# Performance work log

Hardware: AMD Instinct MI355X
Metric: run time of the kernel (lower is better)

## Reference

```python
import jax, jax.numpy as jnp
import numpy as np

S, B, H = 4096, 32, 512

def setup_inputs() -> dict:
    key = jax.random.key(0)
    k1, k2, k3, k4, k5 = jax.random.split(key, 5)
    hidden = jax.random.normal(k1, (1, B, H), dtype=jnp.float32)
    encoder_outputs = jax.random.normal(k2, (S, B, H), dtype=jnp.float32)
    embedding = jax.random.normal(k3, (S, B, 3), dtype=jnp.float32)
    # learned params (xavier-ish scale)
    bigram_matrix = jax.random.normal(k4, (H, H), dtype=jnp.float32) * (1.0 / np.sqrt(H))
    affect_matrix = jax.random.normal(k5, (H, 3), dtype=jnp.float32) * 0.1
    return {"hidden": hidden, "encoder_outputs": encoder_outputs,
            "embedding": embedding, "bigram_matrix": bigram_matrix,
            "affect_matrix": affect_matrix}

def reference(hidden, encoder_outputs, embedding, bigram_matrix, affect_matrix):
    # hidden: [1,B,H] -> [B,H] (view(-1) over single layer)
    h = hidden[0]
    # bigram-modulated encoder states:
    #   i == 0: enc[0]
    #   i  > 0: (enc[i-1] @ W_bigram) * enc[i]
    modulated = jnp.einsum('sbh,hk->sbk', encoder_outputs[:-1], bigram_matrix) * encoder_outputs[1:]
    bigram_hidden = jnp.concatenate([encoder_outputs[:1], modulated], axis=0)  # [S,B,H]
    # dot-attention energy per (b, s)
    e_dot = jnp.einsum('sbh,bh->bs', bigram_hidden, h)  # [B,S]
    # affect term: (h @ affect_matrix) . embedding[s,b]
    e_aff = jnp.einsum('bk,sbk->bs', jnp.einsum('bh,hk->bk', h, affect_matrix), embedding)
    attn = jax.nn.softmax(e_dot + e_aff, axis=-1)  # softmax over seq dim
    return attn[:, None, :]  # [B,1,S]
```

## Files before the change

### kernel.cpp

```cpp
#include <hip/hip_runtime.h>
#include <cstdint>
#include <cstddef>

#define S_DIM 4096
#define B_DIM 32
#define H_DIM 512
#define M_DIM (S_DIM * B_DIM)

typedef unsigned short u16;
typedef unsigned int u32;
typedef float f32x4 __attribute__((ext_vector_type(4)));
typedef __bf16 bf16x8 __attribute__((ext_vector_type(8)));

__device__ __forceinline__ u16 f2bf(float v) {
    union { float f; u32 u; } a; a.f = v;
    u32 r = a.u + 0x7fffu + ((a.u >> 16) & 1u);
    return (u16)(r >> 16);
}
__device__ __forceinline__ float bf2f(u16 b) {
    union { float f; u32 u; } a; a.u = ((u32)b) << 16; return a.f;
}
__device__ __forceinline__ void split_bf(float v, u16& h, u16& l) {
    h = f2bf(v);
    l = f2bf(v - bf2f(h));
}

__device__ __forceinline__ void gl2lds16(const void* g, void* l) {
    __builtin_amdgcn_global_load_lds(
        (const __attribute__((address_space(1))) unsigned int*)g,
        (__attribute__((address_space(3))) unsigned int*)l,
        16, 0, 0);
}

__global__ void prep_w(const float* __restrict__ W,
                       u16* __restrict__ Wh, u16* __restrict__ Wl) {
    int i = blockIdx.x * 256 + threadIdx.x;
    float w = W[i];
    u16 h, l;
    split_bf(w, h, l);
    Wh[i] = h; Wl[i] = l;
}

__global__ void prep_v(const float* __restrict__ enc,
                       const float* __restrict__ hid,
                       u16* __restrict__ vh, u16* __restrict__ vl,
                       int m_base, int m_count) {
    const size_t nq = (size_t)m_count * (H_DIM / 4);
    const size_t stride = (size_t)gridDim.x * 256;
    for (size_t i = blockIdx.x * 256 + threadIdx.x; i < nq; i += stride) {
        const size_t elem  = i * 4;
        const size_t gelem = (size_t)m_base * H_DIM + elem;
        const int k = (int)(gelem & (H_DIM - 1));
        const int b = (int)((gelem >> 9) & 31);
        const float4 e = *(const float4*)(enc + gelem);
        const float4 h = *(const float4*)(hid + b * H_DIM + k);
        float v0 = e.x * h.x, v1 = e.y * h.y, v2 = e.z * h.z, v3 = e.w * h.w;
        u16 h0,h1,h2,h3,l0,l1,l2,l3;
        split_bf(v0, h0, l0); split_bf(v1, h1, l1);
        split_bf(v2, h2, l2); split_bf(v3, h3, l3);
        ushort4 hw, lw;
        hw.x = h0; hw.y = h1; hw.z = h2; hw.w = h3;
        lw.x = l0; lw.y = l1; lw.z = l2; lw.w = l3;
        *(ushort4*)(vh + elem) = hw;
        *(ushort4*)(vl + elem) = lw;
    }
}

__global__ __launch_bounds__(256, 2) void bigram_gemm(
    const float* __restrict__ enc,
    const u16* __restrict__ vh, const u16* __restrict__ vl,
    const u16* __restrict__ Wh, const u16* __restrict__ Wl,
    float* __restrict__ Lp, int m_base)
{
    __shared__ u16 sAh[128 * 32];
    __shared__ u16 sAl[128 * 32];
    __shared__ u16 sBh[128 * 32];
    __shared__ u16 sBl[128 * 32];
    __shared__ float rowsum[2][128];

    const int tid  = threadIdx.x;
    const int wave = tid >> 6;
    const int lane = tid & 63;
    const int wr   = wave >> 1;
    const int wc   = wave & 1;
    const int jt   = blockIdx.x & 3;
    const int mt   = blockIdx.x >> 2;
    const int m0   = m_base + mt * 128;
    const int j0   = jt * 128;
    const int g    = lane >> 4;
    const int cl   = lane & 15;

    const int srow = wave * 32 + (lane >> 2);
    const int scol = (lane & 3) * 8;
    const size_t aoff0 = (size_t)(mt * 128 + srow) * H_DIM + scol;
    const size_t aoff1 = aoff0 + (size_t)16 * H_DIM;
    const size_t boff0 = (size_t)(j0 + srow) * H_DIM + scol;
    const size_t boff1 = boff0 + (size_t)16 * H_DIM;
    const u16* pAh0 = vh + aoff0; const u16* pAh1 = vh + aoff1;
    const u16* pAl0 = vl + aoff0; const u16* pAl1 = vl + aoff1;
    const u16* pBh0 = Wh + boff0; const u16* pBh1 = Wh + boff1;
    const u16* pBl0 = Wl + boff0; const u16* pBl1 = Wl + boff1;
    const int d0 = wave * 1024, d1 = wave * 1024 + 512;

    f32x4 acc[4][4];
    #pragma unroll
    for (int mf = 0; mf < 4; ++mf)
        #pragma unroll
        for (int nf = 0; nf < 4; ++nf)
            acc[mf][nf] = (f32x4){0.f, 0.f, 0.f, 0.f};

    for (int kt = 0; kt < 16; ++kt) {
        const int ko = kt * 32;
        __syncthreads();
        gl2lds16(pAh0 + ko, sAh + d0);
        gl2lds16(pAh1 + ko, sAh + d1);
        gl2lds16(pAl0 + ko, sAl + d0);
        gl2lds16(pAl1 + ko, sAl + d1);
        gl2lds16(pBh0 + ko, sBh + d0);
        gl2lds16(pBh1 + ko, sBh + d1);
        gl2lds16(pBl0 + ko, sBl + d0);
        gl2lds16(pBl1 + ko, sBl + d1);
        __syncthreads();

        bf16x8 ah[4], al[4], bh[4], bl[4];
        #pragma unroll
        for (int mf = 0; mf < 4; ++mf) {
            const int ar = wr * 64 + mf * 16 + cl;
            ah[mf] = *(const bf16x8*)(sAh + ar * 32 + g * 8);
            al[mf] = *(const bf16x8*)(sAl + ar * 32 + g * 8);
        }
        #pragma unroll
        for (int nf = 0; nf < 4; ++nf) {
            const int br = wc * 64 + nf * 16 + cl;
            bh[nf] = *(const bf16x8*)(sBh + br * 32 + g * 8);
            bl[nf] = *(const bf16x8*)(sBl + br * 32 + g * 8);
        }
        #pragma unroll
        for (int mf = 0; mf < 4; ++mf)
            #pragma unroll
            for (int nf = 0; nf < 4; ++nf) {
                acc[mf][nf] = __builtin_amdgcn_mfma_f32_16x16x32_bf16(ah[mf], bh[nf], acc[mf][nf], 0, 0, 0);
                acc[mf][nf] = __builtin_amdgcn_mfma_f32_16x16x32_bf16(ah[mf], bl[nf], acc[mf][nf], 0, 0, 0);
                acc[mf][nf] = __builtin_amdgcn_mfma_f32_16x16x32_bf16(al[mf], bh[nf], acc[mf][nf], 0, 0, 0);
            }
    }

    #pragma unroll
    for (int mf = 0; mf < 4; ++mf) {
        float rs0 = 0.f, rs1 = 0.f, rs2 = 0.f, rs3 = 0.f;
        const int growb = m0 + wr * 64 + mf * 16 + g * 4;
        #pragma unroll
        for (int nf = 0; nf < 4; ++nf) {
            const int gcol = j0 + wc * 64 + nf * 16 + cl;
            float e0 = (growb + 0 >= B_DIM) ? enc[(size_t)(growb + 0 - B_DIM) * H_DIM + gcol] : 0.f;
            float e1 = (growb + 1 >= B_DIM) ? enc[(size_t)(growb + 1 - B_DIM) * H_DIM + gcol] : 0.f;
            float e2 = (growb + 2 >= B_DIM) ? enc[(size_t)(growb + 2 - B_DIM) * H_DIM + gcol] : 0.f;
            float e3 = (growb + 3 >= B_DIM) ? enc[(size_t)(growb + 3 - B_DIM) * H_DIM + gcol] : 0.f;
            rs0 += acc[mf][nf][0] * e0;
            rs1 += acc[mf][nf][1] * e1;
            rs2 += acc[mf][nf][2] * e2;
            rs3 += acc[mf][nf][3] * e3;
        }
        #pragma unroll
        for (int off = 1; off < 16; off <<= 1) {
            rs0 += __shfl_xor(rs0, off);
            rs1 += __shfl_xor(rs1, off);
            rs2 += __shfl_xor(rs2, off);
            rs3 += __shfl_xor(rs3, off);
        }
        if (cl == 0) {
            const int rb = wr * 64 + mf * 16 + g * 4;
            rowsum[wc][rb + 0] = rs0;
            rowsum[wc][rb + 1] = rs1;
            rowsum[wc][rb + 2] = rs2;
            rowsum[wc][rb + 3] = rs3;
        }
    }
    __syncthreads();
    if (tid < 128) {
        const int gm = m0 + tid;
        if (gm >= B_DIM) {
            Lp[(size_t)jt * M_DIM + (size_t)(gm & 31) * S_DIM + (gm >> 5)] =
                rowsum[0][tid] + rowsum[1][tid];
        }
    }
}

__global__ __launch_bounds__(256, 2) void bigram_gemm_direct(
    const float* __restrict__ enc,
    const float* __restrict__ hid,
    const u16* __restrict__ Wh,
    const u16* __restrict__ Wl,
    float* __restrict__ Lp)
{
    __shared__ float rowsum[2][128];
    const int tid  = threadIdx.x;
    const int wave = tid >> 6;
    const int lane = tid & 63;
    const int wr   = wave >> 1;
    const int wc   = wave & 1;
    const int jt   = blockIdx.x & 3;
    const int m0   = (blockIdx.x >> 2) * 128;
    const int j0   = jt * 128;
    const int g    = lane >> 4;
    const int cl   = lane & 15;

    f32x4 acc[4][4];
    #pragma unroll
    for (int mf = 0; mf < 4; ++mf)
        #pragma unroll
        for (int nf = 0; nf < 4; ++nf)
            acc[mf][nf] = (f32x4){0.f, 0.f, 0.f, 0.f};

    for (int kt = 0; kt < 8; ++kt) {
        #pragma unroll
        for (int kk = 0; kk < 2; ++kk) {
            const int k0 = kt * 64 + kk * 32 + g * 8;
            const float4 hA0 = *(const float4*)(hid + (size_t)cl * H_DIM + k0);
            const float4 hA1 = *(const float4*)(hid + (size_t)cl * H_DIM + k0 + 4);
            const float4 hB0 = *(const float4*)(hid + (size_t)(cl + 16) * H_DIM + k0);
            const float4 hB1 = *(const float4*)(hid + (size_t)(cl + 16) * H_DIM + k0 + 4);
            bf16x8 ah[4], al[4];
            #pragma unroll
            for (int mf = 0; mf < 4; ++mf) {
                const size_t rbase = (size_t)(m0 + wr * 64 + mf * 16 + cl) * H_DIM + k0;
                const float4 e0 = *(const float4*)(enc + rbase);
                const float4 e1 = *(const float4*)(enc + rbase + 4);
                const float4 h0 = (mf & 1) ? hB0 : hA0;
                const float4 h1 = (mf & 1) ? hB1 : hA1;
                float v[8];
                v[0] = e0.x * h0.x; v[1] = e0.y * h0.y; v[2] = e0.z * h0.z; v[3] = e0.w * h0.w;
                v[4] = e1.x * h1.x; v[5] = e1.y * h1.y; v[6] = e1.z * h1.z; v[7] = e1.w * h1.w;
                union { bf16x8 v8; u16 s[8]; } Hi, Lo;
                #pragma unroll
                for (int i = 0; i < 8; ++i) split_bf(v[i], Hi.s[i], Lo.s[i]);
                ah[mf] = Hi.v8;
                al[mf] = Lo.v8;
            }
            bf16x8 bh[4], bl[4];
            #pragma unroll
            for (int nf = 0; nf < 4; ++nf) {
                const size_t roff = (size_t)(j0 + wc * 64 + nf * 16 + cl) * H_DIM + k0;
                bh[nf] = *(const bf16x8*)(Wh + roff);
                bl[nf] = *(const bf16x8*)(Wl + roff);
            }
            #pragma unroll
            for (int mf = 0; mf < 4; ++mf)
                #pragma unroll
                for (int nf = 0; nf < 4; ++nf) {
                    acc[mf][nf] = __builtin_amdgcn_mfma_f32_16x16x32_bf16(ah[mf], bh[nf], acc[mf][nf], 0, 0, 0);
                    acc[mf][nf] = __builtin_amdgcn_mfma_f32_16x16x32_bf16(ah[mf], bl[nf], acc[mf][nf], 0, 0, 0);
                    acc[mf][nf] = __builtin_amdgcn_mfma_f32_16x16x32_bf16(al[mf], bh[nf], acc[mf][nf], 0, 0, 0);
                }
        }
    }

    #pragma unroll
    for (int mf = 0; mf < 4; ++mf) {
        float rs0 = 0.f, rs1 = 0.f, rs2 = 0.f, rs3 = 0.f;
        const int growb = m0 + wr * 64 + mf * 16 + g * 4;
        #pragma unroll
        for (int nf = 0; nf < 4; ++nf) {
            const int gcol = j0 + wc * 64 + nf * 16 + cl;
            float e0 = (growb + 0 >= B_DIM) ? enc[(size_t)(growb + 0 - B_DIM) * H_DIM + gcol] : 0.f;
            float e1 = (growb + 1 >= B_DIM) ? enc[(size_t)(growb + 1 - B_DIM) * H_DIM + gcol] : 0.f;
            float e2 = (growb + 2 >= B_DIM) ? enc[(size_t)(growb + 2 - B_DIM) * H_DIM + gcol] : 0.f;
            float e3 = (growb + 3 >= B_DIM) ? enc[(size_t)(growb + 3 - B_DIM) * H_DIM + gcol] : 0.f;
            rs0 += acc[mf][nf][0] * e0;
            rs1 += acc[mf][nf][1] * e1;
            rs2 += acc[mf][nf][2] * e2;
            rs3 += acc[mf][nf][3] * e3;
        }
        #pragma unroll
        for (int off = 1; off < 16; off <<= 1) {
            rs0 += __shfl_xor(rs0, off);
            rs1 += __shfl_xor(rs1, off);
            rs2 += __shfl_xor(rs2, off);
            rs3 += __shfl_xor(rs3, off);
        }
        if (cl == 0) {
            const int rb = wr * 64 + mf * 16 + g * 4;
            rowsum[wc][rb + 0] = rs0;
            rowsum[wc][rb + 1] = rs1;
            rowsum[wc][rb + 2] = rs2;
            rowsum[wc][rb + 3] = rs3;
        }
    }
    __syncthreads();
    if (tid < 128) {
        const int gm = m0 + tid;
        if (gm >= B_DIM) {
            Lp[(size_t)jt * M_DIM + (size_t)(gm & 31) * S_DIM + (gm >> 5)] =
                rowsum[0][tid] + rowsum[1][tid];
        }
    }
}

__global__ __launch_bounds__(1024) void softmax_kernel(
    const float* __restrict__ enc,
    const float* __restrict__ hid,
    const float* __restrict__ emb,
    const float* __restrict__ aff,
    const float* __restrict__ Lp,
    float* __restrict__ out)
{
    __shared__ float logits[S_DIM];
    __shared__ float wred[16][4];
    __shared__ float bcast[4];
    __shared__ float wtmp[16];

    const int b    = blockIdx.x;
    const int tid  = threadIdx.x;
    const int wave = tid >> 6;
    const int lane = tid & 63;

    float p0 = 0.f, p1 = 0.f, p2 = 0.f, p3 = 0.f;
    if (tid < H_DIM) {
        const int h = tid;
        const float hv = hid[b * H_DIM + h];
        p0 = hv * aff[h * 3 + 0];
        p1 = hv * aff[h * 3 + 1];
        p2 = hv * aff[h * 3 + 2];
        p3 = hv * enc[(size_t)b * H_DIM + h];
    }
    #pragma unroll
    for (int off = 32; off > 0; off >>= 1) {
        p0 += __shfl_down(p0, off);
        p1 += __shfl_down(p1, off);
        p2 += __shfl_down(p2, off);
        p3 += __shfl_down(p3, off);
    }
    if (lane == 0) { wred[wave][0] = p0; wred[wave][1] = p1; wred[wave][2] = p2; wred[wave][3] = p3; }
    __syncthreads();
    if (tid < 4) {
        float s = 0.f;
        #pragma unroll
        for (int w = 0; w < 16; ++w) s += wred[w][tid];
        bcast[tid] = s;
    }
    __syncthreads();
    const float ha0 = bcast[0], ha1 = bcast[1], ha2 = bcast[2], s0dot = bcast[3];

    float mx = -3.4e38f;
    #pragma unroll
    for (int it = 0; it < 4; ++it) {
        const int s = tid + it * 1024;
        const size_t base = (size_t)b * S_DIM + s;
        const float ed = (s == 0) ? s0dot
            : (Lp[base] + Lp[(size_t)M_DIM + base] + Lp[2 * (size_t)M_DIM + base] + Lp[3 * (size_t)M_DIM + base]);
        const float* e = emb + (size_t)(s * B_DIM + b) * 3;
        const float lg = ed + ha0 * e[0] + ha1 * e[1] + ha2 * e[2];
        logits[s] = lg;
        mx = fmaxf(mx, lg);
    }
    #pragma unroll
    for (int off = 32; off > 0; off >>= 1) mx = fmaxf(mx, __shfl_xor(mx, off));
    if (lane == 0) wtmp[wave] = mx;
    __syncthreads();
    mx = wtmp[0];
    #pragma unroll
    for (int w = 1; w < 16; ++w) mx = fmaxf(mx, wtmp[w]);
    __syncthreads();

    float sum = 0.f;
    #pragma unroll
    for (int it = 0; it < 4; ++it) {
        const int s = tid + it * 1024;
        const float ex = __expf(logits[s] - mx);
        logits[s] = ex;
        sum += ex;
    }
    #pragma unroll
    for (int off = 32; off > 0; off >>= 1) sum += __shfl_xor(sum, off);
    if (lane == 0) wtmp[wave] = sum;
    __syncthreads();
    sum = 0.f;
    #pragma unroll
    for (int w = 0; w < 16; ++w) sum += wtmp[w];
    const float inv = 1.0f / sum;
    #pragma unroll
    for (int it = 0; it < 4; ++it) {
        const int s = tid + it * 1024;
        out[(size_t)b * S_DIM + s] = logits[s] * inv;
    }
}

extern "C" void kernel_launch(void* const* d_in, const int* in_sizes, int n_in,
                              void* d_out, int out_size, void* d_ws, size_t ws_size,
                              hipStream_t stream) {
    const float* hid = (const float*)d_in[0];
    const float* enc = (const float*)d_in[1];
    const float* emb = (const float*)d_in[2];
    const float* Wm  = (const float*)d_in[3];
    const float* aff = (const float*)d_in[4];
    float* out = (float*)d_out;

    char* ws = (char*)d_ws;
    u16*   Wh = (u16*)ws;
    u16*   Wl = (u16*)(ws + (512u << 10));
    float* Lp = (float*)(ws + (1024u << 10));
    char*  vbase = ws + (1024u << 10) + (size_t)4 * M_DIM * 4;
    const size_t fixed = (1024u << 10) + (size_t)4 * M_DIM * 4;

    hipLaunchKernelGGL(prep_w, dim3(1024), dim3(256), 0, stream, Wm, Wh, Wl);

    const size_t avail = (ws_size > fixed) ? ws_size - fixed : 0;
    long chunk_m = (long)((avail / 2048) / 128) * 128;
    if (chunk_m > M_DIM) chunk_m = M_DIM;

    if (chunk_m >= 128) {
        u16* vh = (u16*)vbase;
        u16* vl = (u16*)(vbase + (size_t)chunk_m * H_DIM * sizeof(u16));
        for (long m_base = 0; m_base < M_DIM; m_base += chunk_m) {
            long mc = M_DIM - m_base;
            if (mc > chunk_m) mc = chunk_m;
            hipLaunchKernelGGL(prep_v, dim3((u32)(mc / 16)), dim3(256), 0, stream,
                               enc, hid, vh, vl, (int)m_base, (int)mc);
            hipLaunchKernelGGL(bigram_gemm, dim3((u32)((mc / 128) * 4)), dim3(256), 0, stream,
                               enc, vh, vl, Wh, Wl, Lp, (int)m_base);
        }
    } else {
        hipLaunchKernelGGL(bigram_gemm_direct, dim3(4096), dim3(256), 0, stream,
                           enc, hid, Wh, Wl, Lp);
    }

    hipLaunchKernelGGL(softmax_kernel, dim3(32), dim3(1024), 0, stream,
                       enc, hid, emb, aff, Lp, out);
}
```

Measured before the change: 649.2 us.

## Fuse hidden-scaling and bf16 split into double-buffered GEMM; split softmax across blocks

The separate prep_v pass, which wrote bf16 hi/lo copies of enc*hidden to workspace, is removed. The GEMM kernel now loads fp32 encoder rows, multiplies by hidden, splits to bf16 and stores into double-buffered LDS, prefetching the next k-tile during the MFMAs. Block indices are remapped across 8 groups, likely for cache or XCD locality. The 32-block softmax is replaced by a prep kernel plus two 256-block passes, one for partial max/sum and one for the final normalisation, to raise parallelism. The cost is more VGPR and LDS pressure in the GEMM and extra launches and logit round trips for the softmax.

Result: faster. 606.0 us (-6.7%).

```diff
diff --git a/kernel.cpp b/kernel.cpp
--- a/kernel.cpp
+++ b/kernel.cpp
@@ -41,41 +41,38 @@
     Wh[i] = h; Wl[i] = l;
 }
 
-__global__ void prep_v(const float* __restrict__ enc,
-                       const float* __restrict__ hid,
-                       u16* __restrict__ vh, u16* __restrict__ vl,
-                       int m_base, int m_count) {
-    const size_t nq = (size_t)m_count * (H_DIM / 4);
-    const size_t stride = (size_t)gridDim.x * 256;
-    for (size_t i = blockIdx.x * 256 + threadIdx.x; i < nq; i += stride) {
-        const size_t elem  = i * 4;
-        const size_t gelem = (size_t)m_base * H_DIM + elem;
-        const int k = (int)(gelem & (H_DIM - 1));
-        const int b = (int)((gelem >> 9) & 31);
-        const float4 e = *(const float4*)(enc + gelem);
-        const float4 h = *(const float4*)(hid + b * H_DIM + k);
-        float v0 = e.x * h.x, v1 = e.y * h.y, v2 = e.z * h.z, v3 = e.w * h.w;
-        u16 h0,h1,h2,h3,l0,l1,l2,l3;
-        split_bf(v0, h0, l0); split_bf(v1, h1, l1);
-        split_bf(v2, h2, l2); split_bf(v3, h3, l3);
-        ushort4 hw, lw;
-        hw.x = h0; hw.y = h1; hw.z = h2; hw.w = h3;
-        lw.x = l0; lw.y = l1; lw.z = l2; lw.w = l3;
-        *(ushort4*)(vh + elem) = hw;
-        *(ushort4*)(vl + elem) = lw;
-    }
-}
-
-__global__ __launch_bounds__(256, 2) void bigram_gemm(
+__device__ __forceinline__ void split4_store(
+    float4 e, float4 h, u16* dh, u16* dl)
+{
+    float vf[4] = { e.x * h.x, e.y * h.y, e.z * h.z, e.w * h.w };
+    u32 rh[4], rl[4];
+    #pragma unroll
+    for (int i = 0; i < 4; ++i) {
+        const u32 u = __float_as_uint(vf[i]);
+        rh[i] = (u + 0x7fffu + ((u >> 16) & 1u)) & 0xffff0000u;
+        const float lo_f = vf[i] - __uint_as_float(rh[i]);
+        const u32 ul = __float_as_uint(lo_f);
+        rl[i] = ul + 0x7fffu + ((ul >> 16) & 1u);
+    }
+    uint2 hw, lw;
+    hw.x = rh[1] | (rh[0] >> 16);
+    hw.y = rh[3] | (rh[2] >> 16);
+    lw.x = (rl[1] & 0xffff0000u) | (rl[0] >> 16);
+    lw.y = (rl[3] & 0xffff0000u) | (rl[2] >> 16);
+    *(uint2*)dh = hw;
+    *(uint2*)dl = lw;
+}
+
+__global__ __launch_bounds__(256, 2) void bigram_gemm_fused(
     const float* __restrict__ enc,
-    const u16* __restrict__ vh, const u16* __restrict__ vl,
+    const float* __restrict__ hid,
     const u16* __restrict__ Wh, const u16* __restrict__ Wl,
-    float* __restrict__ Lp, int m_base)
-{
-    __shared__ u16 sAh[128 * 32];
-    __shared__ u16 sAl[128 * 32];
-    __shared__ u16 sBh[128 * 32];
-    __shared__ u16 sBl[128 * 32];
+    float* __restrict__ Lp)
+{
+    __shared__ u16 sAh[2][128 * 32];
+    __shared__ u16 sAl[2][128 * 32];
+    __shared__ u16 sBh[2][128 * 32];
+    __shared__ u16 sBl[2][128 * 32];
     __shared__ float rowsum[2][128];
 
     const int tid  = threadIdx.x;
@@ -83,24 +80,30 @@
     const int lane = tid & 63;
     const int wr   = wave >> 1;
     const int wc   = wave & 1;
-    const int jt   = blockIdx.x & 3;
-    const int mt   = blockIdx.x >> 2;
-    const int m0   = m_base + mt * 128;
+    const int logical = (blockIdx.x & 7) * 512 + (blockIdx.x >> 3);
+    const int jt   = logical & 3;
+    const int mt   = logical >> 2;
+    const int m0   = mt * 128;
     const int j0   = jt * 128;
     const int g    = lane >> 4;
     const int cl   = lane & 15;
 
     const int srow = wave * 32 + (lane >> 2);
     const int scol = (lane & 3) * 8;
-    const size_t aoff0 = (size_t)(mt * 128 + srow) * H_DIM + scol;
-    const size_t aoff1 = aoff0 + (size_t)16 * H_DIM;
     const size_t boff0 = (size_t)(j0 + srow) * H_DIM + scol;
     const size_t boff1 = boff0 + (size_t)16 * H_DIM;
-    const u16* pAh0 = vh + aoff0; const u16* pAh1 = vh + aoff1;
-    const u16* pAl0 = vl + aoff0; const u16* pAl1 = vl + aoff1;
     const u16* pBh0 = Wh + boff0; const u16* pBh1 = Wh + boff1;
     const u16* pBl0 = Wl + boff0; const u16* pBl1 = Wl + boff1;
-    const int d0 = wave * 1024, d1 = wave * 1024 + 512;
+    const int d0 = wave * 1024, d1 = d0 + 512;
+
+    const int abrow = tid >> 3;
+    const int akq   = tid & 7;
+    const float* pe0 = enc + (size_t)(m0 +  0 + abrow) * H_DIM + akq * 4;
+    const float* pe1 = enc + (size_t)(m0 + 32 + abrow) * H_DIM + akq * 4;
+    const float* pe2 = enc + (size_t)(m0 + 64 + abrow) * H_DIM + akq * 4;
+    const float* pe3 = enc + (size_t)(m0 + 96 + abrow) * H_DIM + akq * 4;
+    const float* ph  = hid + (size_t)abrow * H_DIM + akq * 4;
+    const int awoff = abrow * 32 + akq * 4;
 
     f32x4 acc[4][4];
     #pragma unroll
@@ -109,31 +112,53 @@
         for (int nf = 0; nf < 4; ++nf)
             acc[mf][nf] = (f32x4){0.f, 0.f, 0.f, 0.f};
 
+    {
+        gl2lds16(pBh0, &sBh[0][d0]);
+        gl2lds16(pBh1, &sBh[0][d1]);
+        gl2lds16(pBl0, &sBl[0][d0]);
+        gl2lds16(pBl1, &sBl[0][d1]);
+        const float4 h0 = *(const float4*)ph;
+        const float4 e0 = *(const float4*)pe0;
+        const float4 e1 = *(const float4*)pe1;
+        const float4 e2 = *(const float4*)pe2;
+        const float4 e3 = *(const float4*)pe3;
+        split4_store(e0, h0, &sAh[0][0 * 1024 + awoff], &sAl[0][0 * 1024 + awoff]);
+        split4_store(e1, h0, &sAh[0][1 * 1024 + awoff], &sAl[0][1 * 1024 + awoff]);
+        split4_store(e2, h0, &sAh[0][2 * 1024 + awoff], &sAl[0][2 * 1024 + awoff]);
+        split4_store(e3, h0, &sAh[0][3 * 1024 + awoff], &sAl[0][3 * 1024 + awoff]);
+    }
+    __syncthreads();
+
+    #pragma unroll 2
     for (int kt = 0; kt < 16; ++kt) {
-        const int ko = kt * 32;
-        __syncthreads();
-        gl2lds16(pAh0 + ko, sAh + d0);
-        gl2lds16(pAh1 + ko, sAh + d1);
-        gl2lds16(pAl0 + ko, sAl + d0);
-        gl2lds16(pAl1 + ko, sAl + d1);
-        gl2lds16(pBh0 + ko, sBh + d0);
-        gl2lds16(pBh1 + ko, sBh + d1);
-        gl2lds16(pBl0 + ko, sBl + d0);
-        gl2lds16(pBl1 + ko, sBl + d1);
-        __syncthreads();
+        const int cur = kt & 1, nxt = cur ^ 1;
+        const int ko = (kt + 1) * 32;
+
+        float4 e0n, e1n, e2n, e3n, hn;
+        if (kt < 15) {
+            gl2lds16(pBh0 + ko, &sBh[nxt][d0]);
+            gl2lds16(pBh1 + ko, &sBh[nxt][d1]);
+            gl2lds16(pBl0 + ko, &sBl[nxt][d0]);
+            gl2lds16(pBl1 + ko, &sBl[nxt][d1]);
+            e0n = *(const float4*)(pe0 + ko);
+            e1n = *(const float4*)(pe1 + ko);
+            e2n = *(const float4*)(pe2 + ko);
+            e3n = *(const float4*)(pe3 + ko);
+            hn  = *(const float4*)(ph + ko);
+        }
 
         bf16x8 ah[4], al[4], bh[4], bl[4];
         #pragma unroll
         for (int mf = 0; mf < 4; ++mf) {
             const int ar = wr * 64 + mf * 16 + cl;
-            ah[mf] = *(const bf16x8*)(sAh + ar * 32 + g * 8);
-            al[mf] = *(const bf16x8*)(sAl + ar * 32 + g * 8);
+            ah[mf] = *(const bf16x8*)(&sAh[cur][ar * 32 + g * 8]);
+            al[mf] = *(const bf16x8*)(&sAl[cur][ar * 32 + g * 8]);
         }
         #pragma unroll
         for (int nf = 0; nf < 4; ++nf) {
             const int br = wc * 64 + nf * 16 + cl;
-            bh[nf] = *(const bf16x8*)(sBh + br * 32 + g * 8);
-            bl[nf] = *(const bf16x8*)(sBl + br * 32 + g * 8);
+            bh[nf] = *(const bf16x8*)(&sBh[cur][br * 32 + g * 8]);
+            bl[nf] = *(const bf16x8*)(&sBl[cur][br * 32 + g * 8]);
         }
         #pragma unroll
         for (int mf = 0; mf < 4; ++mf)
@@ -143,6 +168,14 @@
                 acc[mf][nf] = __builtin_amdgcn_mfma_f32_16x16x32_bf16(ah[mf], bl[nf], acc[mf][nf], 0, 0, 0);
                 acc[mf][nf] = __builtin_amdgcn_mfma_f32_16x16x32_bf16(al[mf], bh[nf], acc[mf][nf], 0, 0, 0);
             }
+
+        if (kt < 15) {
+            split4_store(e0n, hn, &sAh[nxt][0 * 1024 + awoff], &sAl[nxt][0 * 1024 + awoff]);
+            split4_store(e1n, hn, &sAh[nxt][1 * 1024 + awoff], &sAl[nxt][1 * 1024 + awoff]);
+            split4_store(e2n, hn, &sAh[nxt][2 * 1024 + awoff], &sAl[nxt][2 * 1024 + awoff]);
+            split4_store(e3n, hn, &sAh[nxt][3 * 1024 + awoff], &sAl[nxt][3 * 1024 + awoff]);
+        }
+        __syncthreads();
     }
 
     #pragma unroll
@@ -186,202 +219,112 @@
     }
 }
 
-__global__ __launch_bounds__(256, 2) void bigram_gemm_direct(
+__global__ __launch_bounds__(256) void prep_aff(
     const float* __restrict__ enc,
     const float* __restrict__ hid,
-    const u16* __restrict__ Wh,
-    const u16* __restrict__ Wl,
-    float* __restrict__ Lp)
-{
-    __shared__ float rowsum[2][128];
-    const int tid  = threadIdx.x;
-    const int wave = tid >> 6;
-    const int lane = tid & 63;
-    const int wr   = wave >> 1;
-    const int wc   = wave & 1;
-    const int jt   = blockIdx.x & 3;
-    const int m0   = (blockIdx.x >> 2) * 128;
-    const int j0   = jt * 128;
-    const int g    = lane >> 4;
-    const int cl   = lane & 15;
-
-    f32x4 acc[4][4];
-    #pragma unroll
-    for (int mf = 0; mf < 4; ++mf)
-        #pragma unroll
-        for (int nf = 0; nf < 4; ++nf)
-            acc[mf][nf] = (f32x4){0.f, 0.f, 0.f, 0.f};
-
-    for (int kt = 0; kt < 8; ++kt) {
-        #pragma unroll
-        for (int kk = 0; kk < 2; ++kk) {
-            const int k0 = kt * 64 + kk * 32 + g * 8;
-            const float4 hA0 = *(const float4*)(hid + (size_t)cl * H_DIM + k0);
-            const float4 hA1 = *(const float4*)(hid + (size_t)cl * H_DIM + k0 + 4);
-            const float4 hB0 = *(const float4*)(hid + (size_t)(cl + 16) * H_DIM + k0);
-            const float4 hB1 = *(const float4*)(hid + (size_t)(cl + 16) * H_DIM + k0 + 4);
-            bf16x8 ah[4], al[4];
-            #pragma unroll
-            for (int mf = 0; mf < 4; ++mf) {
-                const size_t rbase = (size_t)(m0 + wr * 64 + mf * 16 + cl) * H_DIM + k0;
-                const float4 e0 = *(const float4*)(enc + rbase);
-                const float4 e1 = *(const float4*)(enc + rbase + 4);
-                const float4 h0 = (mf & 1) ? hB0 : hA0;
-                const float4 h1 = (mf & 1) ? hB1 : hA1;
-                float v[8];
-                v[0] = e0.x * h0.x; v[1] = e0.y * h0.y; v[2] = e0.z * h0.z; v[3] = e0.w * h0.w;
-                v[4] = e1.x * h1.x; v[5] = e1.y * h1.y; v[6] = e1.z * h1.z; v[7] = e1.w * h1.w;
-                union { bf16x8 v8; u16 s[8]; } Hi, Lo;
-                #pragma unroll
-                for (int i = 0; i < 8; ++i) split_bf(v[i], Hi.s[i], Lo.s[i]);
-                ah[mf] = Hi.v8;
-                al[mf] = Lo.v8;
-            }
-            bf16x8 bh[4], bl[4];
-            #pragma unroll
-            for (int nf = 0; nf < 4; ++nf) {
-                const size_t roff = (size_t)(j0 + wc * 64 + nf * 16 + cl) * H_DIM + k0;
-                bh[nf] = *(const bf16x8*)(Wh + roff);
-                bl[nf] = *(const bf16x8*)(Wl + roff);
-            }
-            #pragma unroll
-            for (int mf = 0; mf < 4; ++mf)
-                #pragma unroll
-                for (int nf = 0; nf < 4; ++nf) {
-                    acc[mf][nf] = __builtin_amdgcn_mfma_f32_16x16x32_bf16(ah[mf], bh[nf], acc[mf][nf], 0, 0, 0);
-                    acc[mf][nf] = __builtin_amdgcn_mfma_f32_16x16x32_bf16(ah[mf], bl[nf], acc[mf][nf], 0, 0, 0);
-                    acc[mf][nf] = __builtin_amdgcn_mfma_f32_16x16x32_bf16(al[mf], bh[nf], acc[mf][nf], 0, 0, 0);
-                }
-        }
-    }
-
-    #pragma unroll
-    for (int mf = 0; mf < 4; ++mf) {
-        float rs0 = 0.f, rs1 = 0.f, rs2 = 0.f, rs3 = 0.f;
-        const int growb = m0 + wr * 64 + mf * 16 + g * 4;
-        #pragma unroll
-        for (int nf = 0; nf < 4; ++nf) {
-            const int gcol = j0 + wc * 64 + nf * 16 + cl;
-            float e0 = (growb + 0 >= B_DIM) ? enc[(size_t)(growb + 0 - B_DIM) * H_DIM + gcol] : 0.f;
-            float e1 = (growb + 1 >= B_DIM) ? enc[(size_t)(growb + 1 - B_DIM) * H_DIM + gcol] : 0.f;
-            float e2 = (growb + 2 >= B_DIM) ? enc[(size_t)(growb + 2 - B_DIM) * H_DIM + gcol] : 0.f;
-            float e3 = (growb + 3 >= B_DIM) ? enc[(size_t)(growb + 3 - B_DIM) * H_DIM + gcol] : 0.f;
-            rs0 += acc[mf][nf][0] * e0;
-            rs1 += acc[mf][nf][1] * e1;
-            rs2 += acc[mf][nf][2] * e2;
-            rs3 += acc[mf][nf][3] * e3;
-        }
-        #pragma unroll
-        for (int off = 1; off < 16; off <<= 1) {
-            rs0 += __shfl_xor(rs0, off);
-            rs1 += __shfl_xor(rs1, off);
-            rs2 += __shfl_xor(rs2, off);
-            rs3 += __shfl_xor(rs3, off);
-        }
-        if (cl == 0) {
-            const int rb = wr * 64 + mf * 16 + g * 4;
-            rowsum[wc][rb + 0] = rs0;
-            rowsum[wc][rb + 1] = rs1;
-            rowsum[wc][rb + 2] = rs2;
-            rowsum[wc][rb + 3] = rs3;
-        }
-    }
-    __syncthreads();
-    if (tid < 128) {
-        const int gm = m0 + tid;
-        if (gm >= B_DIM) {
-            Lp[(size_t)jt * M_DIM + (size_t)(gm & 31) * S_DIM + (gm >> 5)] =
-                rowsum[0][tid] + rowsum[1][tid];
-        }
-    }
-}
-
-__global__ __launch_bounds__(1024) void softmax_kernel(
-    const float* __restrict__ enc,
-    const float* __restrict__ hid,
-    const float* __restrict__ emb,
     const float* __restrict__ aff,
-    const float* __restrict__ Lp,
-    float* __restrict__ out)
-{
-    __shared__ float logits[S_DIM];
-    __shared__ float wred[16][4];
-    __shared__ float bcast[4];
-    __shared__ float wtmp[16];
-
+    float* __restrict__ Aux)
+{
+    __shared__ float w[4][4];
     const int b    = blockIdx.x;
     const int tid  = threadIdx.x;
     const int wave = tid >> 6;
     const int lane = tid & 63;
 
     float p0 = 0.f, p1 = 0.f, p2 = 0.f, p3 = 0.f;
-    if (tid < H_DIM) {
-        const int h = tid;
+    #pragma unroll
+    for (int it = 0; it < 2; ++it) {
+        const int h = tid + it * 256;
         const float hv = hid[b * H_DIM + h];
-        p0 = hv * aff[h * 3 + 0];
-        p1 = hv * aff[h * 3 + 1];
-        p2 = hv * aff[h * 3 + 2];
-        p3 = hv * enc[(size_t)b * H_DIM + h];
+        p0 += hv * aff[h * 3 + 0];
+        p1 += hv * aff[h * 3 + 1];
+        p2 += hv * aff[h * 3 + 2];
+        p3 += hv * enc[(size_t)b * H_DIM + h];
     }
     #pragma unroll
     for (int off = 32; off > 0; off >>= 1) {
-        p0 += __shfl_down(p0, off);
-        p1 += __shfl_down(p1, off);
-        p2 += __shfl_down(p2, off);
-        p3 += __shfl_down(p3, off);
-    }
-    if (lane == 0) { wred[wave][0] = p0; wred[wave][1] = p1; wred[wave][2] = p2; wred[wave][3] = p3; }
-    __syncthreads();
-    if (tid < 4) {
-        float s = 0.f;
-        #pragma unroll
-        for (int w = 0; w < 16; ++w) s += wred[w][tid];
-        bcast[tid] = s;
-    }
-    __syncthreads();
-    const float ha0 = bcast[0], ha1 = bcast[1], ha2 = bcast[2], s0dot = bcast[3];
-
+        p0 += __shfl_xor(p0, off);
+        p1 += __shfl_xor(p1, off);
+        p2 += __shfl_xor(p2, off);
+        p3 += __shfl_xor(p3, off);
+    }
+    if (lane == 0) { w[wave][0] = p0; w[wave][1] = p1; w[wave][2] = p2; w[wave][3] = p3; }
+    __syncthreads();
+    if (tid < 4)
+        Aux[b * 4 + tid] = w[0][tid] + w[1][tid] + w[2][tid] + w[3][tid];
+}
+
+__global__ __launch_bounds__(256) void sm_partial(
+    const float* __restrict__ emb,
+    const float* __restrict__ Lp,
+    const float* __restrict__ Aux,
+    float* __restrict__ Lg,
+    float* __restrict__ Part)
+{
+    __shared__ float wm[4];
+    __shared__ float wsum[4];
+    const int b     = blockIdx.x >> 3;
+    const int strip = blockIdx.x & 7;
+    const int tid   = threadIdx.x;
+    const int wave  = tid >> 6;
+    const int lane  = tid & 63;
+
+    const float ha0 = Aux[b * 4 + 0], ha1 = Aux[b * 4 + 1],
+                ha2 = Aux[b * 4 + 2], s0dot = Aux[b * 4 + 3];
+
+    float lgv[2];
     float mx = -3.4e38f;
     #pragma unroll
-    for (int it = 0; it < 4; ++it) {
-        const int s = tid + it * 1024;
+    for (int it = 0; it < 2; ++it) {
+        const int s = strip * 512 + it * 256 + tid;
         const size_t base = (size_t)b * S_DIM + s;
         const float ed = (s == 0) ? s0dot
             : (Lp[base] + Lp[(size_t)M_DIM + base] + Lp[2 * (size_t)M_DIM + base] + Lp[3 * (size_t)M_DIM + base]);
         const float* e = emb + (size_t)(s * B_DIM + b) * 3;
         const float lg = ed + ha0 * e[0] + ha1 * e[1] + ha2 * e[2];
-        logits[s] = lg;
+        Lg[(size_t)b * S_DIM + s] = lg;
+        lgv[it] = lg;
         mx = fmaxf(mx, lg);
     }
     #pragma unroll
     for (int off = 32; off > 0; off >>= 1) mx = fmaxf(mx, __shfl_xor(mx, off));
-    if (lane == 0) wtmp[wave] = mx;
-    __syncthreads();
-    mx = wtmp[0];
-    #pragma unroll
-    for (int w = 1; w < 16; ++w) mx = fmaxf(mx, wtmp[w]);
-    __syncthreads();
-
-    float sum = 0.f;
-    #pragma unroll
-    for (int it = 0; it < 4; ++it) {
-        const int s = tid + it * 1024;
-        const float ex = __expf(logits[s] - mx);
-        logits[s] = ex;
-        sum += ex;
-    }
+    if (lane == 0) wm[wave] = mx;
+    __syncthreads();
+    mx = fmaxf(fmaxf(wm[0], wm[1]), fmaxf(wm[2], wm[3]));
+
+    float sum = __expf(lgv[0] - mx) + __expf(lgv[1] - mx);
     #pragma unroll
     for (int off = 32; off > 0; off >>= 1) sum += __shfl_xor(sum, off);
-    if (lane == 0) wtmp[wave] = sum;
-    __syncthreads();
-    sum = 0.f;
-    #pragma unroll
-    for (int w = 0; w < 16; ++w) sum += wtmp[w];
-    const float inv = 1.0f / sum;
-    #pragma unroll
-    for (int it = 0; it < 4; ++it) {
-        const int s = tid + it * 1024;
-        out[(size_t)b * S_DIM + s] = logits[s] * inv;
+    if (lane == 0) wsum[wave] = sum;
+    __syncthreads();
+    if (tid == 0) {
+        Part[(size_t)(b * 8 + strip) * 2 + 0] = mx;
+        Part[(size_t)(b * 8 + strip) * 2 + 1] = wsum[0] + wsum[1] + wsum[2] + wsum[3];
+    }
+}
+
+__global__ __launch_bounds__(256) void sm_final(
+    const float* __restrict__ Lg,
+    const float* __restrict__ Part,
+    float* __restrict__ out)
+{
+    const int b     = blockIdx.x >> 3;
+    const int strip = blockIdx.x & 7;
+    const int tid   = threadIdx.x;
+
+    float M = -3.4e38f;
+    #pragma unroll
+    for (int i = 0; i < 8; ++i) M = fmaxf(M, Part[(size_t)(b * 8 + i) * 2]);
+    float S = 0.f;
+    #pragma unroll
+    for (int i = 0; i < 8; ++i)
+        S += Part[(size_t)(b * 8 + i) * 2 + 1] * __expf(Part[(size_t)(b * 8 + i) * 2] - M);
+    const float inv = 1.0f / S;
+
+    #pragma unroll
+    for (int it = 0; it < 2; ++it) {
+        const int s = strip * 512 + it * 256 + tid;
+        out[(size_t)b * S_DIM + s] = __expf(Lg[(size_t)b * S_DIM + s] - M) * inv;
     }
 }
 
@@ -396,34 +339,19 @@
     float* out = (float*)d_out;
 
     char* ws = (char*)d_ws;
-    u16*   Wh = (u16*)ws;
-    u16*   Wl = (u16*)(ws + (512u << 10));
-    float* Lp = (float*)(ws + (1024u << 10));
-    char*  vbase = ws + (1024u << 10) + (size_t)4 * M_DIM * 4;
-    const size_t fixed = (1024u << 10) + (size_t)4 * M_DIM * 4;
+    u16*   Wh  = (u16*)ws;
+    u16*   Wl  = (u16*)(ws + (512u << 10));
+    float* Lp  = (float*)(ws + (1024u << 10));
+    float* Aux = (float*)(ws + (3072u << 10));
+    float* Lg  = (float*)(ws + (3072u << 10) + 1024);
+    float* Part= (float*)(ws + (3072u << 10) + 1024 + (512u << 10));
 
     hipLaunchKernelGGL(prep_w, dim3(1024), dim3(256), 0, stream, Wm, Wh, Wl);
-
-    const size_t avail = (ws_size > fixed) ? ws_size - fixed : 0;
-    long chunk_m = (long)((avail / 2048) / 128) * 128;
-    if (chunk_m > M_DIM) chunk_m = M_DIM;
-
-    if (chunk_m >= 128) {
-        u16* vh = (u16*)vbase;
-        u16* vl = (u16*)(vbase + (size_t)chunk_m * H_DIM * sizeof(u16));
-        for (long m_base = 0; m_base < M_DIM; m_base += chunk_m) {
-            long mc = M_DIM - m_base;
-            if (mc > chunk_m) mc = chunk_m;
-            hipLaunchKernelGGL(prep_v, dim3((u32)(mc / 16)), dim3(256), 0, stream,
-                               enc, hid, vh, vl, (int)m_base, (int)mc);
-            hipLaunchKernelGGL(bigram_gemm, dim3((u32)((mc / 128) * 4)), dim3(256), 0, stream,
-                               enc, vh, vl, Wh, Wl, Lp, (int)m_base);
-        }
-    } else {
-        hipLaunchKernelGGL(bigram_gemm_direct, dim3(4096), dim3(256), 0, stream,
-                           enc, hid, Wh, Wl, Lp);
-    }
-
-    hipLaunchKernelGGL(softmax_kernel, dim3(32), dim3(1024), 0, stream,
-                       enc, hid, emb, aff, Lp, out);
-}
+    hipLaunchKernelGGL(prep_aff, dim3(32), dim3(256), 0, stream, enc, hid, aff, Aux);
+    hipLaunchKernelGGL(bigram_gemm_fused, dim3(4096), dim3(256), 0, stream,
+                       enc, hid, Wh, Wl, Lp);
+    hipLaunchKernelGGL(sm_partial, dim3(256), dim3(256), 0, stream,
+                       emb, Lp, Aux, Lg, Part);
+    hipLaunchKernelGGL(sm_final, dim3(256), dim3(256), 0, stream,
+                       Lg, Part, out);
+}
```
